# Optimization experiments

Hardware: AMD Instinct MI355X
Metric: run time of the kernel (lower is better)

The kernel has to match this reference:

```python
import jax, jax.numpy as jnp
import numpy as np
from jax import lax

# Production-scale RPN detection-head config
B, FH, FW, NA = 8, 200, 200, 9      # batch, fmap h, fmap w, anchors/cell
H, W = 800, 800                      # image dims
N = FH * FW * NA                     # 360k anchors per image
NMS_THR = 0.7
MIN_SIZE = 1e-3


def _make_anchors():
    scales = np.array([32.0, 64.0, 128.0])
    ratios = np.array([0.5, 1.0, 2.0])
    ws = (scales[:, None] * np.sqrt(1.0 / ratios)[None, :]).reshape(-1)  # [NA]
    hs = (scales[:, None] * np.sqrt(ratios)[None, :]).reshape(-1)
    sy, sx = H / FH, W / FW
    cx = (np.arange(FW) + 0.5) * sx
    cy = (np.arange(FH) + 0.5) * sy
    cxg, cyg = np.meshgrid(cx, cy)                     # [FH,FW]
    cxg = cxg[..., None]; cyg = cyg[..., None]         # [FH,FW,1]
    a = np.stack([cxg - ws / 2, cyg - hs / 2, cxg + ws / 2, cyg + hs / 2], axis=-1)
    return jnp.asarray(a.reshape(-1, 4), jnp.float32)  # [N,4] xyxy


def setup_inputs() -> dict:
    key = jax.random.key(0)
    k1, k2 = jax.random.split(key)
    cls_logits = jax.random.normal(k1, (B, N, 1), jnp.float32)
    reg_deltas = jax.random.normal(k2, (B, N, 4), jnp.float32) * 0.1  # sane exp(dw)
    anchors = jnp.broadcast_to(_make_anchors()[None], (B, N, 4))
    return {
        "cls_logits": cls_logits,
        "reg_deltas": reg_deltas,
        "anchors": anchors,
        "keep_pre_nms": 1000,
        "keep_post_nms": 300,
    }


def _offsets2boxes(deltas, anchors):
    aw = anchors[:, 2] - anchors[:, 0]
    ah = anchors[:, 3] - anchors[:, 1]
    acx = anchors[:, 0] + 0.5 * aw
    acy = anchors[:, 1] + 0.5 * ah
    cx = deltas[:, 0] * aw + acx
    cy = deltas[:, 1] * ah + acy
    w = jnp.exp(deltas[:, 2]) * aw
    h = jnp.exp(deltas[:, 3]) * ah
    return jnp.stack([cx - 0.5 * w, cy - 0.5 * h, cx + 0.5 * w, cy + 0.5 * h], axis=-1)


def _iou_matrix(b):
    area = (b[:, 2] - b[:, 0]) * (b[:, 3] - b[:, 1])
    lt = jnp.maximum(b[:, None, :2], b[None, :, :2])
    rb = jnp.minimum(b[:, None, 2:], b[None, :, 2:])
    wh = jnp.clip(rb - lt, 0.0)
    inter = wh[..., 0] * wh[..., 1]
    return inter / (area[:, None] + area[None, :] - inter + 1e-9)


def _detect_one(logit, delta, anc, pre, post):
    scores = jax.nn.sigmoid(logit.reshape(-1))             # [N]
    boxes = _offsets2boxes(delta.reshape(-1, 4), anc)      # [N,4]
    s, idx = lax.top_k(scores, pre)                        # sorted desc
    b = boxes[idx]                                         # [pre,4]
    # clip to image
    b = jnp.stack([
        jnp.clip(b[:, 0], 0.0, W), jnp.clip(b[:, 1], 0.0, H),
        jnp.clip(b[:, 2], 0.0, W), jnp.clip(b[:, 3], 0.0, H)], axis=-1)
    valid = ((b[:, 2] - b[:, 0]) >= MIN_SIZE) & ((b[:, 3] - b[:, 1]) >= MIN_SIZE)
    # greedy NMS on score-sorted boxes (mask-based, fixed shapes)
    iou = _iou_matrix(lax.stop_gradient(b))                # [pre,pre]
    j = jnp.arange(pre)

    def body(keep, i):
        sup = (iou[i] > NMS_THR) & (j > i) & keep[i]
        return keep & ~sup, None

    keep, _ = lax.scan(body, valid, jnp.arange(pre))
    # compact first `post` kept detections into fixed [post,5], zero-padded
    dets = jnp.concatenate([b, s[:, None]], axis=-1)       # [pre,5]
    rank = jnp.cumsum(keep) - 1
    tgt = jnp.where(keep & (rank < post), rank, post)
    out = jnp.zeros((post + 1, 5), dets.dtype).at[tgt].set(dets)[:post]
    return out


def reference(cls_logits, reg_deltas, anchors, keep_pre_nms, keep_post_nms):
    f = lambda l, d, a: _detect_one(l, d, a, keep_pre_nms, keep_post_nms)
    return jax.vmap(f)(cls_logits, reg_deltas, anchors)    # [B,post,5]
```

## Files before the change

kernel.cpp:

```cpp
#include <hip/hip_runtime.h>
#include <stdint.h>
#include <math.h>

typedef unsigned long long u64;
typedef unsigned int u32;

#define NPI   360000
#define B_IMG 8
#define PRE   1000
#define POST  300
#define CAP   4096
#define NMSF  0.7f
#define IMG_W 800.0f
#define IMG_H 800.0f

#define NBIN    8192
#define KSHIFT  19
#define CHUNK_H 36
#define F4PB_H  (NPI / 4 / CHUNK_H)
#define CHUNK_C 48
#define F4PB_C  (NPI / 4 / CHUNK_C)
#define EPB_C   (NPI / CHUNK_C)
#define LBUF    1024

#define CNT_OFF    0
#define THRESH_OFF 128
#define VALID_OFF  256
#define RHIST_OFF  4096
#define ZERO_BYTES 266240
#define BOX_OFF    266240
#define SCORE_OFF  394240
#define CAND_OFF   426240
#define MASK_OFF   688384

__device__ __forceinline__ u32 fkey(float f) {
  u32 u = __float_as_uint(f);
  return (u & 0x80000000u) ? ~u : (u | 0x80000000u);
}
__device__ __forceinline__ u64 rl64(u64 v, int lane) {
  u32 lo = (u32)__builtin_amdgcn_readlane((int)(u32)v, lane);
  u32 hi = (u32)__builtin_amdgcn_readlane((int)(u32)(v >> 32), lane);
  return ((u64)hi << 32) | lo;
}
__device__ __forceinline__ u64 sx64(u64 v, int m) {
  u32 lo = (u32)__shfl_xor((int)(u32)v, m, 64);
  u32 hi = (u32)__shfl_xor((int)(u32)(v >> 32), m, 64);
  return ((u64)hi << 32) | lo;
}

__global__ __launch_bounds__(256) void k_hist(const float* __restrict__ logits,
                                              u32* __restrict__ rhist) {
  __shared__ u32 h[NBIN];
  const int img = blockIdx.y, c = blockIdx.x;
  for (int i = threadIdx.x; i < NBIN; i += 256) h[i] = 0;
  __syncthreads();
  const float4* L = (const float4*)(logits + (size_t)img * NPI) + (size_t)c * F4PB_H;
  for (int i = threadIdx.x; i < F4PB_H; i += 256) {
    float4 v = L[i];
    atomicAdd(&h[fkey(v.x) >> KSHIFT], 1u);
    atomicAdd(&h[fkey(v.y) >> KSHIFT], 1u);
    atomicAdd(&h[fkey(v.z) >> KSHIFT], 1u);
    atomicAdd(&h[fkey(v.w) >> KSHIFT], 1u);
  }
  __syncthreads();
  u32* R = rhist + img * NBIN;
  for (int i = threadIdx.x; i < NBIN; i += 256) {
    u32 cn = h[i];
    if (cn) atomicAdd(&R[i], cn);
  }
}

__global__ __launch_bounds__(1024) void k_select(const u32* __restrict__ rhist,
                                                 int* __restrict__ thresh) {
  const int img = blockIdx.x;
  const int t = threadIdx.x;
  const int lane = t & 63, w = t >> 6;
  const uint4* H4 = (const uint4*)(rhist + img * NBIN);
  uint4 v0 = H4[2 * t], v1 = H4[2 * t + 1];
  u32 binc[8] = {v0.x, v0.y, v0.z, v0.w, v1.x, v1.y, v1.z, v1.w};
  u32 s = 0;
#pragma unroll
  for (int b = 0; b < 8; b++) s += binc[b];
  u32 suf = s;
#pragma unroll
  for (int off = 1; off < 64; off <<= 1) {
    u32 o = (u32)__shfl_down((int)suf, off, 64);
    if (lane + off < 64) suf += o;
  }
  __shared__ u32 wtot[16];
  if (lane == 0) wtot[w] = suf;
  __syncthreads();
  u32 wsuf = 0;
  for (int ww = w + 1; ww < 16; ww++) wsuf += wtot[ww];
  u32 suffix_incl = suf + wsuf;
  u32 s_excl = suffix_incl - s;
  if (suffix_incl >= (u32)PRE && s_excl < (u32)PRE) {
    u32 cum = s_excl;
    int bin = 8 * t;
#pragma unroll
    for (int b = 7; b >= 0; b--) {
      cum += binc[b];
      if (cum >= (u32)PRE) { bin = 8 * t + b; break; }
    }
    thresh[img] = bin;
  }
}

__global__ __launch_bounds__(256) void k_compact(const float* __restrict__ logits,
                                                 const int* __restrict__ thresh,
                                                 u32* __restrict__ cnt,
                                                 u64* __restrict__ cand) {
  __shared__ u64 buf[LBUF];
  __shared__ u32 bcnt;
  __shared__ u32 gbase;
  const int img = blockIdx.y, c = blockIdx.x;
  const int tb  = thresh[img];
  if (threadIdx.x == 0) bcnt = 0;
  __syncthreads();
  const float4* L = (const float4*)(logits + (size_t)img * NPI) + (size_t)c * F4PB_C;
  const int ebase = c * EPB_C;
  for (int i = threadIdx.x; i < F4PB_C; i += 256) {
    float4 v = L[i];
    float xs[4] = {v.x, v.y, v.z, v.w};
#pragma unroll
    for (int q = 0; q < 4; q++) {
      float x = xs[q];
      if ((int)(fkey(x) >> KSHIFT) >= tb) {
        float ef = (float)exp(-(double)x);
        float sg = 1.0f / (1.0f + ef);
        u32 e = (u32)(ebase + 4 * i + q);
        u32 p = atomicAdd(&bcnt, 1u);
        if (p < LBUF)
          buf[p] = ((u64)fkey(sg) << 32) | (u64)(0xFFFFFFFFu - e);
      }
    }
  }
  __syncthreads();
  if (threadIdx.x == 0) {
    u32 m = bcnt < LBUF ? bcnt : LBUF;
    bcnt = m;
    gbase = atomicAdd(&cnt[img], m);
  }
  __syncthreads();
  const u32 m = bcnt, gb = gbase;
  for (u32 j = threadIdx.x; j < m; j += 256) {
    u32 pos = gb + j;
    if (pos < CAP) cand[img * CAP + pos] = buf[j];
  }
}

#define RB 8
__device__ __forceinline__ void emit_row(
    int img, int row, u64 key,
    const float* __restrict__ deltas, const float* __restrict__ anchors,
    float4* __restrict__ boxes, float* __restrict__ scores, u64* __restrict__ validw) {
  u32 hi  = (u32)(key >> 32);
  u32 idx = 0xFFFFFFFFu - (u32)(key & 0xFFFFFFFFu);
  u32 su  = (hi & 0x80000000u) ? (hi ^ 0x80000000u) : ~hi;
  float sc = __uint_as_float(su);
  size_t off = (size_t)img * NPI + idx;
  float4 d = ((const float4*)deltas)[off];
  float4 a = ((const float4*)anchors)[off];
  float aw = a.z - a.x, ah = a.w - a.y;
  float acx = a.x + 0.5f * aw, acy = a.y + 0.5f * ah;
  float cx = d.x * aw + acx, cy = d.y * ah + acy;
  float w = expf(d.z) * aw, h = expf(d.w) * ah;
  float x1 = cx - 0.5f * w, y1 = cy - 0.5f * h;
  float x2 = cx + 0.5f * w, y2 = cy + 0.5f * h;
  x1 = fminf(fmaxf(x1, 0.f), IMG_W);
  y1 = fminf(fmaxf(y1, 0.f), IMG_H);
  x2 = fminf(fmaxf(x2, 0.f), IMG_W);
  y2 = fminf(fmaxf(y2, 0.f), IMG_H);
  boxes[img * PRE + row]  = make_float4(x1, y1, x2, y2);
  scores[img * PRE + row] = sc;
  if (((x2 - x1) >= 1e-3f) && ((y2 - y1) >= 1e-3f))
    atomicOr(&validw[img * 16 + (row >> 6)], 1ull << (row & 63));
}

__global__ __launch_bounds__(256) void k_rank(
    const float* __restrict__ deltas, const float* __restrict__ anchors,
    const u32* __restrict__ cnt, const u64* __restrict__ cand,
    float4* __restrict__ boxes, float* __restrict__ scores, u64* __restrict__ validw) {
  __shared__ u64 skey[CAP];
  const int img = blockIdx.y;
  int n = (int)cnt[img];
  if (n > CAP) n = CAP;
  for (int i = threadIdx.x; i < n; i += 256) skey[i] = cand[img * CAP + i];
  __syncthreads();
  const int r0 = blockIdx.x * 256 + threadIdx.x;
  const int r1 = r0 + RB * 256;
  u64 k0 = (r0 < n) ? skey[r0] : 0ull;
  u64 k1 = (r1 < n) ? skey[r1] : 0ull;
  int c0 = 0, c1 = 0;
  for (int j = 0; j < n; j++) {
    u64 kj = skey[j];
    c0 += (kj > k0);
    c1 += (kj > k1);
  }
  if (r0 < n && c0 < PRE) emit_row(img, c0, k0, deltas, anchors, boxes, scores, validw);
  if (r1 < n && c1 < PRE) emit_row(img, c1, k1, deltas, anchors, boxes, scores, validw);
}

__global__ __launch_bounds__(1024) void k_iou(const float4* __restrict__ boxes,
                                              u64* __restrict__ mask) {
  __shared__ float4 sb[1024];
  __shared__ float  sa[1024];
  const int img = blockIdx.y;
  const int tid = threadIdx.x;
  {
    float4 b = (tid < PRE) ? boxes[img * PRE + tid]
                           : make_float4(0.f, 0.f, 0.f, 0.f);
    sb[tid] = b;
    sa[tid] = (b.z - b.x) * (b.w - b.y);
  }
  __syncthreads();
  const int lane = tid & 63;
  const int wv   = tid >> 6;
  const int i    = blockIdx.x * 64 + lane;
  const bool rowok = (i < PRE);
  const float4 bi = sb[blockIdx.x * 64 + lane];
  const float  ai = sa[blockIdx.x * 64 + lane];
  const int cbase = wv << 6;
  u64 bits = 0;
#pragma unroll
  for (int k = 0; k < 64; k++) {
    int c = cbase + k;
    float4 bc = sb[c];
    float ac  = sa[c];
    float ltx = fmaxf(bi.x, bc.x), lty = fmaxf(bi.y, bc.y);
    float rbx = fminf(bi.z, bc.z), rby = fminf(bi.w, bc.w);
    float iw = fmaxf(rbx - ltx, 0.f), ih = fmaxf(rby - lty, 0.f);
    float inter = iw * ih;
    float iou = inter / (ai + ac - inter + 1e-9f);
    bits |= (iou > NMSF) ? (1ull << k) : 0ull;
  }
  int d = i - cbase;
  u64 gtmask = (d < 0) ? ~0ull : ((d >= 63) ? 0ull : (~0ull << (d + 1)));
  int rem = PRE - cbase;
  u64 tmask = (rem >= 64) ? ~0ull : ((rem <= 0) ? 0ull : ((1ull << rem) - 1ull));
  bits &= gtmask & tmask;
  if (rowok) mask[((size_t)img * PRE + i) * 16 + wv] = bits;
}

#define LDSROWS 496
#define NMS_T   320
__global__ __launch_bounds__(NMS_T) void k_nms(
    const u64* __restrict__ mask, const u64* __restrict__ validw,
    const float4* __restrict__ boxes, const float* __restrict__ scores,
    float* __restrict__ out) {
  __shared__ u64 smask[LDSROWS * 16];
  __shared__ int skeeplist[POST];
  __shared__ int skept;
  const int img = blockIdx.x;
  const int tid = threadIdx.x;
  const u64* M = mask + (size_t)img * PRE * 16;
  u64 diag[16];
  if (tid < 64) {
#pragma unroll
    for (int cc = 0; cc < 16; cc++) {
      int row = cc * 64 + tid;
      diag[cc] = (row < PRE) ? M[(size_t)row * 16 + cc] : 0ull;
    }
  }
  for (int e = tid; e < LDSROWS * 16; e += NMS_T) smask[e] = M[e];
  __syncthreads();
  if (tid < 64) {
    const int lane = tid;
    const int w = lane & 15, g = lane >> 4;
    u64 rem = ~0ull;
    if (lane < 16) {
      rem = ~validw[img * 16 + lane];
      if (lane == 15) rem |= 0xFFFFFF0000000000ull;
    }
    int kept = 0;
#pragma unroll
    for (int cc = 0; cc < 16; cc++) {
      u64 alive = ~rl64(rem, cc);
      int kept0 = kept;
      while (alive != 0ull && kept < POST) {
        int r = __builtin_ctzll(alive);
        if (lane == 0) skeeplist[kept] = cc * 64 + r;
        kept++;
        u64 sup = rl64(diag[cc], r);
        alive &= ~sup;
        alive &= ~(1ull << r);
      }
      int nc = kept - kept0;
      if (nc > 0 && kept < POST && cc < 15) {
        u64 part = 0;
        for (int j = g; j < nc; j += 4) {
          int row = skeeplist[kept0 + j];
          part |= (row < LDSROWS) ? smask[row * 16 + w] : M[(size_t)row * 16 + w];
        }
        part |= sx64(part, 16);
        part |= sx64(part, 32);
        rem |= part;
      }
      if (kept >= POST) break;
    }
    if (lane == 0) skept = kept;
  }
  __syncthreads();
  if (tid < POST) {
    float4 bx = make_float4(0.f, 0.f, 0.f, 0.f);
    float  sc = 0.f;
    if (tid < skept) {
      int i = skeeplist[tid];
      bx = boxes[img * PRE + i];
      sc = scores[img * PRE + i];
    }
    float* o = out + ((size_t)img * POST + tid) * 5;
    o[0] = bx.x; o[1] = bx.y; o[2] = bx.z; o[3] = bx.w; o[4] = sc;
  }
}

extern "C" void kernel_launch(void* const* d_in, const int* in_sizes, int n_in,
                              void* d_out, int out_size, void* d_ws, size_t ws_size,
                              hipStream_t stream) {
  const float* logits  = (const float*)d_in[0];
  const float* deltas  = (const float*)d_in[1];
  const float* anchors = (const float*)d_in[2];
  float* out = (float*)d_out;
  char* ws = (char*)d_ws;

  u32* cnt      = (u32*)(ws + CNT_OFF);
  int* thresh   = (int*)(ws + THRESH_OFF);
  u64* validw   = (u64*)(ws + VALID_OFF);
  u32* rhist    = (u32*)(ws + RHIST_OFF);
  float4* boxes = (float4*)(ws + BOX_OFF);
  float* scores = (float*)(ws + SCORE_OFF);
  u64* cand     = (u64*)(ws + CAND_OFF);
  u64* mask     = (u64*)(ws + MASK_OFF);

  hipMemsetAsync(ws, 0, ZERO_BYTES, stream);
  dim3 gh(CHUNK_H, B_IMG);
  k_hist<<<gh, 256, 0, stream>>>(logits, rhist);
  k_select<<<B_IMG, 1024, 0, stream>>>(rhist, thresh);
  dim3 gc(CHUNK_C, B_IMG);
  k_compact<<<gc, 256, 0, stream>>>(logits, thresh, cnt, cand);
  dim3 gr(RB, B_IMG);
  k_rank<<<gr, 256, 0, stream>>>(deltas, anchors, cnt, cand, boxes, scores, validw);
  dim3 g2(16, B_IMG);
  k_iou<<<g2, 1024, 0, stream>>>(boxes, mask);
  k_nms<<<B_IMG, NMS_T, 0, stream>>>(mask, validw, boxes, scores, out);
}
```

Measured before the change: 210.2 us.

## Fuse all detection stages into one cooperative persistent kernel with grid syncs

After: 493.9 us. 135% more time.

```diff
diff --git a/kernel.cpp b/kernel.cpp
--- a/kernel.cpp
+++ b/kernel.cpp
@@ -1,6 +1,9 @@
 #include <hip/hip_runtime.h>
+#include <hip/hip_cooperative_groups.h>
 #include <stdint.h>
 #include <math.h>
+
+namespace cg = cooperative_groups;
 
 typedef unsigned long long u64;
 typedef unsigned int u32;
@@ -16,18 +19,16 @@
 
 #define NBIN    8192
 #define KSHIFT  19
-#define CHUNK_H 36
-#define F4PB_H  (NPI / 4 / CHUNK_H)
-#define CHUNK_C 48
-#define F4PB_C  (NPI / 4 / CHUNK_C)
-#define EPB_C   (NPI / CHUNK_C)
+#define HC      64
+#define F4C     1407
+#define NU_HC   (B_IMG * HC)
 #define LBUF    1024
+#define LDSROWS 496
 
 #define CNT_OFF    0
 #define THRESH_OFF 128
 #define VALID_OFF  256
 #define RHIST_OFF  4096
-#define ZERO_BYTES 266240
 #define BOX_OFF    266240
 #define SCORE_OFF  394240
 #define CAND_OFF   426240
@@ -48,108 +49,6 @@
   return ((u64)hi << 32) | lo;
 }
 
-__global__ __launch_bounds__(256) void k_hist(const float* __restrict__ logits,
-                                              u32* __restrict__ rhist) {
-  __shared__ u32 h[NBIN];
-  const int img = blockIdx.y, c = blockIdx.x;
-  for (int i = threadIdx.x; i < NBIN; i += 256) h[i] = 0;
-  __syncthreads();
-  const float4* L = (const float4*)(logits + (size_t)img * NPI) + (size_t)c * F4PB_H;
-  for (int i = threadIdx.x; i < F4PB_H; i += 256) {
-    float4 v = L[i];
-    atomicAdd(&h[fkey(v.x) >> KSHIFT], 1u);
-    atomicAdd(&h[fkey(v.y) >> KSHIFT], 1u);
-    atomicAdd(&h[fkey(v.z) >> KSHIFT], 1u);
-    atomicAdd(&h[fkey(v.w) >> KSHIFT], 1u);
-  }
-  __syncthreads();
-  u32* R = rhist + img * NBIN;
-  for (int i = threadIdx.x; i < NBIN; i += 256) {
-    u32 cn = h[i];
-    if (cn) atomicAdd(&R[i], cn);
-  }
-}
-
-__global__ __launch_bounds__(1024) void k_select(const u32* __restrict__ rhist,
-                                                 int* __restrict__ thresh) {
-  const int img = blockIdx.x;
-  const int t = threadIdx.x;
-  const int lane = t & 63, w = t >> 6;
-  const uint4* H4 = (const uint4*)(rhist + img * NBIN);
-  uint4 v0 = H4[2 * t], v1 = H4[2 * t + 1];
-  u32 binc[8] = {v0.x, v0.y, v0.z, v0.w, v1.x, v1.y, v1.z, v1.w};
-  u32 s = 0;
-#pragma unroll
-  for (int b = 0; b < 8; b++) s += binc[b];
-  u32 suf = s;
-#pragma unroll
-  for (int off = 1; off < 64; off <<= 1) {
-    u32 o = (u32)__shfl_down((int)suf, off, 64);
-    if (lane + off < 64) suf += o;
-  }
-  __shared__ u32 wtot[16];
-  if (lane == 0) wtot[w] = suf;
-  __syncthreads();
-  u32 wsuf = 0;
-  for (int ww = w + 1; ww < 16; ww++) wsuf += wtot[ww];
-  u32 suffix_incl = suf + wsuf;
-  u32 s_excl = suffix_incl - s;
-  if (suffix_incl >= (u32)PRE && s_excl < (u32)PRE) {
-    u32 cum = s_excl;
-    int bin = 8 * t;
-#pragma unroll
-    for (int b = 7; b >= 0; b--) {
-      cum += binc[b];
-      if (cum >= (u32)PRE) { bin = 8 * t + b; break; }
-    }
-    thresh[img] = bin;
-  }
-}
-
-__global__ __launch_bounds__(256) void k_compact(const float* __restrict__ logits,
-                                                 const int* __restrict__ thresh,
-                                                 u32* __restrict__ cnt,
-                                                 u64* __restrict__ cand) {
-  __shared__ u64 buf[LBUF];
-  __shared__ u32 bcnt;
-  __shared__ u32 gbase;
-  const int img = blockIdx.y, c = blockIdx.x;
-  const int tb  = thresh[img];
-  if (threadIdx.x == 0) bcnt = 0;
-  __syncthreads();
-  const float4* L = (const float4*)(logits + (size_t)img * NPI) + (size_t)c * F4PB_C;
-  const int ebase = c * EPB_C;
-  for (int i = threadIdx.x; i < F4PB_C; i += 256) {
-    float4 v = L[i];
-    float xs[4] = {v.x, v.y, v.z, v.w};
-#pragma unroll
-    for (int q = 0; q < 4; q++) {
-      float x = xs[q];
-      if ((int)(fkey(x) >> KSHIFT) >= tb) {
-        float ef = (float)exp(-(double)x);
-        float sg = 1.0f / (1.0f + ef);
-        u32 e = (u32)(ebase + 4 * i + q);
-        u32 p = atomicAdd(&bcnt, 1u);
-        if (p < LBUF)
-          buf[p] = ((u64)fkey(sg) << 32) | (u64)(0xFFFFFFFFu - e);
-      }
-    }
-  }
-  __syncthreads();
-  if (threadIdx.x == 0) {
-    u32 m = bcnt < LBUF ? bcnt : LBUF;
-    bcnt = m;
-    gbase = atomicAdd(&cnt[img], m);
-  }
-  __syncthreads();
-  const u32 m = bcnt, gb = gbase;
-  for (u32 j = threadIdx.x; j < m; j += 256) {
-    u32 pos = gb + j;
-    if (pos < CAP) cand[img * CAP + pos] = buf[j];
-  }
-}
-
-#define RB 8
 __device__ __forceinline__ void emit_row(
     int img, int row, u64 key,
     const float* __restrict__ deltas, const float* __restrict__ anchors,
@@ -177,140 +76,268 @@
     atomicOr(&validw[img * 16 + (row >> 6)], 1ull << (row & 63));
 }
 
-__global__ __launch_bounds__(256) void k_rank(
-    const float* __restrict__ deltas, const float* __restrict__ anchors,
-    const u32* __restrict__ cnt, const u64* __restrict__ cand,
-    float4* __restrict__ boxes, float* __restrict__ scores, u64* __restrict__ validw) {
-  __shared__ u64 skey[CAP];
-  const int img = blockIdx.y;
-  int n = (int)cnt[img];
-  if (n > CAP) n = CAP;
-  for (int i = threadIdx.x; i < n; i += 256) skey[i] = cand[img * CAP + i];
-  __syncthreads();
-  const int r0 = blockIdx.x * 256 + threadIdx.x;
-  const int r1 = r0 + RB * 256;
-  u64 k0 = (r0 < n) ? skey[r0] : 0ull;
-  u64 k1 = (r1 < n) ? skey[r1] : 0ull;
-  int c0 = 0, c1 = 0;
-  for (int j = 0; j < n; j++) {
-    u64 kj = skey[j];
-    c0 += (kj > k0);
-    c1 += (kj > k1);
-  }
-  if (r0 < n && c0 < PRE) emit_row(img, c0, k0, deltas, anchors, boxes, scores, validw);
-  if (r1 < n && c1 < PRE) emit_row(img, c1, k1, deltas, anchors, boxes, scores, validw);
-}
-
-__global__ __launch_bounds__(1024) void k_iou(const float4* __restrict__ boxes,
-                                              u64* __restrict__ mask) {
-  __shared__ float4 sb[1024];
-  __shared__ float  sa[1024];
-  const int img = blockIdx.y;
-  const int tid = threadIdx.x;
-  {
-    float4 b = (tid < PRE) ? boxes[img * PRE + tid]
-                           : make_float4(0.f, 0.f, 0.f, 0.f);
-    sb[tid] = b;
-    sa[tid] = (b.z - b.x) * (b.w - b.y);
-  }
-  __syncthreads();
-  const int lane = tid & 63;
-  const int wv   = tid >> 6;
-  const int i    = blockIdx.x * 64 + lane;
-  const bool rowok = (i < PRE);
-  const float4 bi = sb[blockIdx.x * 64 + lane];
-  const float  ai = sa[blockIdx.x * 64 + lane];
-  const int cbase = wv << 6;
-  u64 bits = 0;
-#pragma unroll
-  for (int k = 0; k < 64; k++) {
-    int c = cbase + k;
-    float4 bc = sb[c];
-    float ac  = sa[c];
-    float ltx = fmaxf(bi.x, bc.x), lty = fmaxf(bi.y, bc.y);
-    float rbx = fminf(bi.z, bc.z), rby = fminf(bi.w, bc.w);
-    float iw = fmaxf(rbx - ltx, 0.f), ih = fmaxf(rby - lty, 0.f);
-    float inter = iw * ih;
-    float iou = inter / (ai + ac - inter + 1e-9f);
-    bits |= (iou > NMSF) ? (1ull << k) : 0ull;
-  }
-  int d = i - cbase;
-  u64 gtmask = (d < 0) ? ~0ull : ((d >= 63) ? 0ull : (~0ull << (d + 1)));
-  int rem = PRE - cbase;
-  u64 tmask = (rem >= 64) ? ~0ull : ((rem <= 0) ? 0ull : ((1ull << rem) - 1ull));
-  bits &= gtmask & tmask;
-  if (rowok) mask[((size_t)img * PRE + i) * 16 + wv] = bits;
-}
-
-#define LDSROWS 496
-#define NMS_T   320
-__global__ __launch_bounds__(NMS_T) void k_nms(
-    const u64* __restrict__ mask, const u64* __restrict__ validw,
-    const float4* __restrict__ boxes, const float* __restrict__ scores,
-    float* __restrict__ out) {
-  __shared__ u64 smask[LDSROWS * 16];
+__global__ __launch_bounds__(256, 2) void k_all(
+    const float* __restrict__ logits, const float* __restrict__ deltas,
+    const float* __restrict__ anchors,
+    u32* __restrict__ rhist, int* __restrict__ thresh, u32* __restrict__ cnt,
+    u64* __restrict__ validw, u64* __restrict__ cand,
+    float4* __restrict__ boxes, float* __restrict__ scores,
+    u64* __restrict__ mask, float* __restrict__ out) {
+  cg::grid_group grid = cg::this_grid();
+  __shared__ alignas(16) char U[65024];
+  __shared__ u32 s_bcnt, s_gbase;
+  __shared__ u32 wtot[4];
   __shared__ int skeeplist[POST];
   __shared__ int skept;
-  const int img = blockIdx.x;
   const int tid = threadIdx.x;
-  const u64* M = mask + (size_t)img * PRE * 16;
-  u64 diag[16];
-  if (tid < 64) {
-#pragma unroll
-    for (int cc = 0; cc < 16; cc++) {
-      int row = cc * 64 + tid;
-      diag[cc] = (row < PRE) ? M[(size_t)row * 16 + cc] : 0ull;
-    }
-  }
-  for (int e = tid; e < LDSROWS * 16; e += NMS_T) smask[e] = M[e];
-  __syncthreads();
-  if (tid < 64) {
-    const int lane = tid;
-    const int w = lane & 15, g = lane >> 4;
-    u64 rem = ~0ull;
-    if (lane < 16) {
-      rem = ~validw[img * 16 + lane];
-      if (lane == 15) rem |= 0xFFFFFF0000000000ull;
-    }
-    int kept = 0;
-#pragma unroll
-    for (int cc = 0; cc < 16; cc++) {
-      u64 alive = ~rl64(rem, cc);
-      int kept0 = kept;
-      while (alive != 0ull && kept < POST) {
-        int r = __builtin_ctzll(alive);
-        if (lane == 0) skeeplist[kept] = cc * 64 + r;
-        kept++;
-        u64 sup = rl64(diag[cc], r);
-        alive &= ~sup;
-        alive &= ~(1ull << r);
-      }
-      int nc = kept - kept0;
-      if (nc > 0 && kept < POST && cc < 15) {
-        u64 part = 0;
-        for (int j = g; j < nc; j += 4) {
-          int row = skeeplist[kept0 + j];
-          part |= (row < LDSROWS) ? smask[row * 16 + w] : M[(size_t)row * 16 + w];
-        }
-        part |= sx64(part, 16);
-        part |= sx64(part, 32);
-        rem |= part;
-      }
-      if (kept >= POST) break;
-    }
-    if (lane == 0) skept = kept;
-  }
-  __syncthreads();
-  if (tid < POST) {
-    float4 bx = make_float4(0.f, 0.f, 0.f, 0.f);
-    float  sc = 0.f;
-    if (tid < skept) {
-      int i = skeeplist[tid];
-      bx = boxes[img * PRE + i];
-      sc = scores[img * PRE + i];
-    }
-    float* o = out + ((size_t)img * POST + tid) * 5;
-    o[0] = bx.x; o[1] = bx.y; o[2] = bx.z; o[3] = bx.w; o[4] = sc;
+  const int bid = blockIdx.x;
+  const int nb  = gridDim.x;
+  const int gid = bid * 256 + tid;
+  const int gsz = nb * 256;
+
+  for (int i = gid; i < B_IMG * NBIN; i += gsz) rhist[i] = 0;
+  if (gid < 8) cnt[gid] = 0;
+  if (gid < 128) validw[gid] = 0ull;
+  grid.sync();
+
+  {
+    u32* h = (u32*)U;
+    for (int u = bid; u < NU_HC; u += nb) {
+      const int img = u >> 6, c = u & 63;
+      for (int i = tid; i < NBIN; i += 256) h[i] = 0;
+      __syncthreads();
+      const float4* L = (const float4*)(logits + (size_t)img * NPI);
+      const int f1 = min((c + 1) * F4C, NPI / 4);
+      for (int i = c * F4C + tid; i < f1; i += 256) {
+        float4 v = L[i];
+        atomicAdd(&h[fkey(v.x) >> KSHIFT], 1u);
+        atomicAdd(&h[fkey(v.y) >> KSHIFT], 1u);
+        atomicAdd(&h[fkey(v.z) >> KSHIFT], 1u);
+        atomicAdd(&h[fkey(v.w) >> KSHIFT], 1u);
+      }
+      __syncthreads();
+      u32* R = rhist + img * NBIN;
+      for (int i = tid; i < NBIN; i += 256) {
+        u32 cn = h[i];
+        if (cn) atomicAdd(&R[i], cn);
+      }
+      __syncthreads();
+    }
+  }
+  grid.sync();
+
+  for (int img = bid; img < B_IMG; img += nb) {
+    const int lane = tid & 63, w = tid >> 6;
+    u32 binc[32];
+    const uint4* H4 = (const uint4*)(rhist + img * NBIN);
+#pragma unroll
+    for (int q = 0; q < 8; q++) {
+      uint4 v = H4[8 * tid + q];
+      binc[4 * q + 0] = v.x; binc[4 * q + 1] = v.y;
+      binc[4 * q + 2] = v.z; binc[4 * q + 3] = v.w;
+    }
+    u32 s = 0;
+#pragma unroll
+    for (int b = 0; b < 32; b++) s += binc[b];
+    u32 suf = s;
+#pragma unroll
+    for (int off = 1; off < 64; off <<= 1) {
+      u32 o = (u32)__shfl_down((int)suf, off, 64);
+      if (lane + off < 64) suf += o;
+    }
+    if (lane == 0) wtot[w] = suf;
+    __syncthreads();
+    u32 wsuf = 0;
+    for (int ww = w + 1; ww < 4; ww++) wsuf += wtot[ww];
+    u32 suffix_incl = suf + wsuf;
+    u32 s_excl = suffix_incl - s;
+    if (suffix_incl >= (u32)PRE && s_excl < (u32)PRE) {
+      u32 cum = s_excl;
+      int bin = 32 * tid;
+      bool found = false;
+#pragma unroll
+      for (int b = 31; b >= 0; b--) {
+        cum += binc[b];
+        if (!found && cum >= (u32)PRE) { bin = 32 * tid + b; found = true; }
+      }
+      thresh[img] = bin;
+    }
+    __syncthreads();
+  }
+  grid.sync();
+
+  {
+    u64* buf = (u64*)U;
+    for (int u = bid; u < NU_HC; u += nb) {
+      const int img = u >> 6, c = u & 63;
+      const int tb = thresh[img];
+      if (tid == 0) s_bcnt = 0;
+      __syncthreads();
+      const float4* L = (const float4*)(logits + (size_t)img * NPI);
+      const int f1 = min((c + 1) * F4C, NPI / 4);
+      for (int i = c * F4C + tid; i < f1; i += 256) {
+        float4 v = L[i];
+        float xs[4] = {v.x, v.y, v.z, v.w};
+#pragma unroll
+        for (int q = 0; q < 4; q++) {
+          float x = xs[q];
+          if ((int)(fkey(x) >> KSHIFT) >= tb) {
+            float ef = (float)exp(-(double)x);
+            float sg = 1.0f / (1.0f + ef);
+            u32 e = (u32)(4 * i + q);
+            u32 p = atomicAdd(&s_bcnt, 1u);
+            if (p < LBUF)
+              buf[p] = ((u64)fkey(sg) << 32) | (u64)(0xFFFFFFFFu - e);
+          }
+        }
+      }
+      __syncthreads();
+      if (tid == 0) {
+        u32 m = s_bcnt < LBUF ? s_bcnt : LBUF;
+        s_bcnt = m;
+        s_gbase = atomicAdd(&cnt[img], m);
+      }
+      __syncthreads();
+      const u32 m = s_bcnt, gb = s_gbase;
+      for (u32 j = tid; j < m; j += 256) {
+        u32 pos = gb + j;
+        if (pos < CAP) cand[img * CAP + pos] = buf[j];
+      }
+      __syncthreads();
+    }
+  }
+  grid.sync();
+
+  {
+    u64* skey = (u64*)U;
+    for (int u = bid; u < 64; u += nb) {
+      const int img = u >> 3, rb = u & 7;
+      int n = (int)cnt[img];
+      if (n > CAP) n = CAP;
+      for (int i = tid; i < n; i += 256) skey[i] = cand[img * CAP + i];
+      __syncthreads();
+      const int r0 = rb * 256 + tid;
+      const int r1 = r0 + 2048;
+      u64 k0 = (r0 < n) ? skey[r0] : 0ull;
+      u64 k1 = (r1 < n) ? skey[r1] : 0ull;
+      int c0 = 0, c1 = 0;
+      for (int j = 0; j < n; j++) {
+        u64 kj = skey[j];
+        c0 += (kj > k0);
+        c1 += (kj > k1);
+      }
+      if (r0 < n && c0 < PRE) emit_row(img, c0, k0, deltas, anchors, boxes, scores, validw);
+      if (r1 < n && c1 < PRE) emit_row(img, c1, k1, deltas, anchors, boxes, scores, validw);
+      __syncthreads();
+    }
+  }
+  grid.sync();
+
+  {
+    float4* sb = (float4*)U;
+    float*  sa = (float*)(U + 16384);
+    for (int u = bid; u < 512; u += nb) {
+      const int v = u >> 2, wq = u & 3;
+      const int img = v >> 4, bx = v & 15;
+      for (int i = tid; i < 1024; i += 256) {
+        float4 b = (i < PRE) ? boxes[img * PRE + i] : make_float4(0.f, 0.f, 0.f, 0.f);
+        sb[i] = b;
+        sa[i] = (b.z - b.x) * (b.w - b.y);
+      }
+      __syncthreads();
+      const int lane = tid & 63;
+      const int wv = wq * 4 + (tid >> 6);
+      const int irow = bx * 64 + lane;
+      const float4 bi = sb[bx * 64 + lane];
+      const float  ai = sa[bx * 64 + lane];
+      const int cbase = wv << 6;
+      u64 bits = 0;
+#pragma unroll
+      for (int k = 0; k < 64; k++) {
+        float4 bc = sb[cbase + k];
+        float ac  = sa[cbase + k];
+        float ltx = fmaxf(bi.x, bc.x), lty = fmaxf(bi.y, bc.y);
+        float rbx = fminf(bi.z, bc.z), rby = fminf(bi.w, bc.w);
+        float iw = fmaxf(rbx - ltx, 0.f), ih = fmaxf(rby - lty, 0.f);
+        float inter = iw * ih;
+        float iou = inter / (ai + ac - inter + 1e-9f);
+        bits |= (iou > NMSF) ? (1ull << k) : 0ull;
+      }
+      int d = irow - cbase;
+      u64 gtmask = (d < 0) ? ~0ull : ((d >= 63) ? 0ull : (~0ull << (d + 1)));
+      int rm = PRE - cbase;
+      u64 tmask = (rm >= 64) ? ~0ull : ((rm <= 0) ? 0ull : ((1ull << rm) - 1ull));
+      bits &= gtmask & tmask;
+      if (irow < PRE) mask[((size_t)img * PRE + irow) * 16 + wv] = bits;
+      __syncthreads();
+    }
+  }
+  grid.sync();
+
+  {
+    u64* smask = (u64*)U;
+    for (int img = bid; img < B_IMG; img += nb) {
+      const u64* M = mask + (size_t)img * PRE * 16;
+      u64 diag[16];
+      if (tid < 64) {
+#pragma unroll
+        for (int cc = 0; cc < 16; cc++) {
+          int row = cc * 64 + tid;
+          diag[cc] = (row < PRE) ? M[(size_t)row * 16 + cc] : 0ull;
+        }
+      }
+      for (int e = tid; e < LDSROWS * 16; e += 256) smask[e] = M[e];
+      __syncthreads();
+      if (tid < 64) {
+        const int lane = tid;
+        const int w = lane & 15, g = lane >> 4;
+        u64 rem = ~0ull;
+        if (lane < 16) {
+          rem = ~validw[img * 16 + lane];
+          if (lane == 15) rem |= 0xFFFFFF0000000000ull;
+        }
+        int kept = 0;
+#pragma unroll
+        for (int cc = 0; cc < 16; cc++) {
+          u64 alive = ~rl64(rem, cc);
+          int kept0 = kept;
+          while (alive != 0ull && kept < POST) {
+            int r = __builtin_ctzll(alive);
+            if (lane == 0) skeeplist[kept] = cc * 64 + r;
+            kept++;
+            u64 sup = rl64(diag[cc], r);
+            alive &= ~sup;
+            alive &= ~(1ull << r);
+          }
+          int nc = kept - kept0;
+          if (nc > 0 && kept < POST && cc < 15) {
+            u64 part = 0;
+            for (int j = g; j < nc; j += 4) {
+              int row = skeeplist[kept0 + j];
+              part |= (row < LDSROWS) ? smask[row * 16 + w] : M[(size_t)row * 16 + w];
+            }
+            part |= sx64(part, 16);
+            part |= sx64(part, 32);
+            rem |= part;
+          }
+          if (kept >= POST) break;
+        }
+        if (lane == 0) skept = kept;
+      }
+      __syncthreads();
+      for (int o = tid; o < POST; o += 256) {
+        float4 bx4 = make_float4(0.f, 0.f, 0.f, 0.f);
+        float sc = 0.f;
+        if (o < skept) {
+          int i = skeeplist[o];
+          bx4 = boxes[img * PRE + i];
+          sc = scores[img * PRE + i];
+        }
+        float* op = out + ((size_t)img * POST + o) * 5;
+        op[0] = bx4.x; op[1] = bx4.y; op[2] = bx4.z; op[3] = bx4.w; op[4] = sc;
+      }
+      __syncthreads();
+    }
   }
 }
 
@@ -332,15 +359,20 @@
   u64* cand     = (u64*)(ws + CAND_OFF);
   u64* mask     = (u64*)(ws + MASK_OFF);
 
-  hipMemsetAsync(ws, 0, ZERO_BYTES, stream);
-  dim3 gh(CHUNK_H, B_IMG);
-  k_hist<<<gh, 256, 0, stream>>>(logits, rhist);
-  k_select<<<B_IMG, 1024, 0, stream>>>(rhist, thresh);
-  dim3 gc(CHUNK_C, B_IMG);
-  k_compact<<<gc, 256, 0, stream>>>(logits, thresh, cnt, cand);
-  dim3 gr(RB, B_IMG);
-  k_rank<<<gr, 256, 0, stream>>>(deltas, anchors, cnt, cand, boxes, scores, validw);
-  dim3 g2(16, B_IMG);
-  k_iou<<<g2, 1024, 0, stream>>>(boxes, mask);
-  k_nms<<<B_IMG, NMS_T, 0, stream>>>(mask, validw, boxes, scores, out);
-}
+  int maxB = 0;
+  hipError_t oe = hipOccupancyMaxActiveBlocksPerMultiprocessor(&maxB, k_all, 256, 0);
+  int G = 512;
+  if (oe == hipSuccess && maxB >= 1) {
+    G = maxB * 256;
+    if (G > 512) G = 512;
+  } else {
+    G = 256;
+  }
+
+  void* args[] = {
+    (void*)&logits, (void*)&deltas, (void*)&anchors,
+    (void*)&rhist, (void*)&thresh, (void*)&cnt, (void*)&validw,
+    (void*)&cand, (void*)&boxes, (void*)&scores, (void*)&mask, (void*)&out
+  };
+  hipLaunchCooperativeKernel((void*)k_all, dim3(G), dim3(256), args, 0, stream);
+}
```
